# Optimization experiments

Measured on AMD Instinct MI355X. Metric: run time of the kernel, lower is better.

## Reference

```python
import jax, jax.numpy as jnp
import numpy as np

N = 25000          # nodes
E = 200000         # edges
MUL = 16           # multiplicity of 0e and 1o in irreps_in/out
NUM_RADIAL = 8
HIDDEN = 64
WNUMEL = 4 * MUL * MUL
PATH_ALPHA = 1.0 / np.sqrt(2.0 * MUL)   # 2 paths feed each output irrep, fan_in=MUL each
INV_SQRT3 = 1.0 / np.sqrt(3.0)          # CG coeff for 1o x 1o -> 0e (component norm)


def setup_inputs() -> dict:
    key = jax.random.key(0)
    ks = jax.random.split(key, 9)
    x = jax.random.normal(ks[0], (N, 4 * MUL), jnp.float32)          # [N, 64] = 16x0e + 16x1o
    edge_attr = jax.random.normal(ks[1], (E, 4), jnp.float32)        # [E, 4]  = 1x0e + 1x1o sh
    edge_length = jax.random.uniform(ks[2], (E,), jnp.float32, 0.0, 5.0)
    edge_src = jax.random.randint(ks[3], (E,), 0, N)
    edge_dst = jax.random.randint(ks[4], (E,), 0, N)
    W1 = jax.random.normal(ks[5], (NUM_RADIAL, HIDDEN), jnp.float32)
    W2 = jax.random.normal(ks[6], (HIDDEN, WNUMEL), jnp.float32)
    L0 = jax.random.normal(ks[7], (MUL, MUL), jnp.float32)           # sc Linear on 0e block
    L1 = jax.random.normal(ks[8], (MUL, MUL), jnp.float32)           # sc Linear on 1o block
    return dict(x=x, edge_attr=edge_attr, edge_length=edge_length,
                edge_src=edge_src, edge_dst=edge_dst, W1=W1, W2=W2, L0=L0, L1=L1)


def reference(x, edge_attr, edge_length, edge_src, edge_dst, W1, W2, L0, L1):
    # ---- radial Gaussian basis (centers linspace(0,5,8), sigma=1) ----
    centers = jnp.linspace(0.0, 5.0, NUM_RADIAL).astype(x.dtype)
    d = edge_length[:, None] - centers[None, :]
    radial = jnp.exp(-0.5 * d * d)                                   # [E, 8]
    # ---- radial MLP -> per-edge TP weights (e3nn FullyConnectedNet, silu) ----
    h = jax.nn.silu(radial @ W1 * (1.0 / np.sqrt(NUM_RADIAL)))       # [E, 64]
    w = (h @ W2 * (1.0 / np.sqrt(HIDDEN))).reshape(E, 4, MUL, MUL)   # [E, 4, 16, 16]
    # ---- gather source node features, split into l=0 and l=1 parts ----
    xj = x[edge_src]                                                  # [E, 64]
    xj0 = xj[:, :MUL]                                                 # [E, 16]
    xj1 = xj[:, MUL:].reshape(E, MUL, 3)                              # [E, 16, 3]
    sh0 = edge_attr[:, 0]                                             # [E]
    sh1 = edge_attr[:, 1:4]                                           # [E, 3]
    # ---- FullyConnectedTensorProduct: 4 CG paths with per-edge weights ----
    m0 = (jnp.einsum('eu,euv->ev', xj0 * sh0[:, None], w[:, 0])
          + INV_SQRT3 * jnp.einsum('euk,ek,euv->ev', xj1, sh1, w[:, 1])) * PATH_ALPHA  # [E,16]
    m1 = (jnp.einsum('eu,ek,euv->evk', xj0, sh1, w[:, 2])
          + jnp.einsum('euk,e,euv->evk', xj1, sh0, w[:, 3])) * PATH_ALPHA              # [E,16,3]
    m_ij = jnp.concatenate([m0, m1.reshape(E, 3 * MUL)], axis=1)      # [E, 64]
    # ---- scatter-add messages to destination nodes ----
    m_i = jax.ops.segment_sum(m_ij, edge_dst, num_segments=N)        # [N, 64]
    # ---- residual self-connection: o3.Linear per-l mixing ----
    x0 = x[:, :MUL]
    x1 = x[:, MUL:].reshape(N, MUL, 3)
    sc0 = x0 @ L0
    sc1 = jnp.einsum('nuk,uv->nvk', x1, L1).reshape(N, 3 * MUL)
    sc = jnp.concatenate([sc0, sc1], axis=1) * (1.0 / np.sqrt(MUL))
    return m_i + sc
```

## Files before the change

kernel.cpp:

```cpp
#include <hip/hip_runtime.h>

#define N_NODES 25000
#define N_EDGES 200000

constexpr int ET = 32;
constexpr int NTILES = 6250;
constexpr int GRID = 512;
constexpr int PL = ET * 17;
constexpr int CTS = 36;

typedef __attribute__((ext_vector_type(8))) _Float16 half8;
typedef __attribute__((ext_vector_type(4))) _Float16 half4;
typedef __attribute__((ext_vector_type(4))) float float4v;

__device__ __forceinline__ void gl_lds16(const void* g, void* l) {
    __builtin_amdgcn_global_load_lds((const __attribute__((address_space(1))) void*)g,
                                     (__attribute__((address_space(3))) void*)l, 16, 0, 0);
}
__device__ __forceinline__ void gl_lds4(const void* g, void* l) {
    __builtin_amdgcn_global_load_lds((const __attribute__((address_space(1))) void*)g,
                                     (__attribute__((address_space(3))) void*)l, 4, 0, 0);
}

__global__ __launch_bounds__(512, 4) void fused_kernel(
    const float* __restrict__ x, const float* __restrict__ edge_attr,
    const float* __restrict__ edge_length, const int* __restrict__ edge_src,
    const int* __restrict__ edge_dst, const float* __restrict__ W1,
    const float* __restrict__ W2, const float* __restrict__ L0,
    const float* __restrict__ L1, float* __restrict__ out) {

    const int t = threadIdx.x;
    const int w = t >> 6;
    const int lane = t & 63;
    const int q = w >> 1;
    const int uh = w & 1;
    const int qm = t & 15;
    const int quad = (t >> 4) & 3;
    const int eL = t >> 4;
    const int uL = t & 15;

    __shared__ __attribute__((aligned(16))) _Float16 lds_h16[ET * 72];
    __shared__ __attribute__((aligned(16))) float lds_cfT[3][16][CTS];
    __shared__ __attribute__((aligned(16))) float lds_cf3T[3][16][CTS];
    __shared__ __attribute__((aligned(16))) float lds_xch[12 * PL];
    __shared__ __attribute__((aligned(16))) float lds_w1t[64 * 8];
    __shared__ __attribute__((aligned(16))) float l0[256], l1[256];
    __shared__ __attribute__((aligned(16))) float lds_xj[2][ET * 64];
    __shared__ __attribute__((aligned(16))) float lds_ea[2][ET * 4];
    __shared__ __attribute__((aligned(16))) float lds_len[2][ET];
    __shared__ __attribute__((aligned(16))) int   lds_dst[2][ET];
    __shared__ __attribute__((aligned(16))) int   lds_srcb[2][ET];

    half8 bfr[8][2];
    {
        float scale = 0.0220970869f;
        if (q == 1) scale *= 0.5773502692f;
        const int kr = quad * 8;
        #pragma unroll
        for (int up = 0; up < 8; ++up) {
            const int col = q * 256 + (uh * 8 + up) * 16 + qm;
            #pragma unroll
            for (int kf = 0; kf < 2; ++kf) {
                half8 f;
                #pragma unroll
                for (int j = 0; j < 8; ++j) {
                    const int k = kf * 32 + kr + j;
                    f[j] = (_Float16)(W2[k * 1024 + col] * scale);
                }
                bfr[up][kf] = f;
            }
        }
    }
    lds_w1t[(t & 63) * 8 + (t >> 6)] = W1[t];
    if (t < 256) l0[t] = L0[t];
    else         l1[t - 256] = L1[t - 256];

    int T = blockIdx.x;
    if (w == 0 && lane < ET) gl_lds4(edge_src + T * ET + lane, &lds_srcb[1][0]);
    __syncthreads();
    {
        const int e4 = (w << 2) + (lane >> 4);
        const int src = lds_srcb[1][e4];
        gl_lds16(x + src * 64 + (lane & 15) * 4, &lds_xj[0][w * 256]);
    }
    if (w == 0 && lane < ET) gl_lds16(edge_attr + 4 * (T * ET + lane), &lds_ea[0][0]);
    if (w == 1 && lane < ET) gl_lds4(edge_length + T * ET + lane, &lds_len[0][0]);
    if (w == 2 && lane < ET) gl_lds4(edge_dst + T * ET + lane, &lds_dst[0][0]);
    if (w == 3 && lane < ET) {
        const int Tn = (T + GRID < NTILES) ? T + GRID : T;
        gl_lds4(edge_src + Tn * ET + lane, &lds_srcb[0][0]);
    }

    {
        const bool is0 = lane < 16;
        const int qq = lane - 16;
        const int v = is0 ? lane : qq / 3;
        const int k = is0 ? 0 : qq - 3 * v;
        const float* mat = is0 ? l0 : l1;
        for (int n = blockIdx.x * 8 + w; n < N_NODES; n += GRID * 8) {
            const float xv = x[n * 64 + lane];
            float s = 0.f;
            #pragma unroll
            for (int u = 0; u < 16; ++u) {
                const int sel = is0 ? u : 16 + 3 * u + k;
                s = fmaf(__shfl(xv, sel), mat[u * 16 + v], s);
            }
            atomicAdd(out + n * 64 + lane, 0.25f * s);
        }
    }
    __syncthreads();

    int p = 0;
    while (true) {
        {
            const float sh0 = lds_ea[p][eL * 4 + 0];
            const float s1x = lds_ea[p][eL * 4 + 1];
            const float s1y = lds_ea[p][eL * 4 + 2];
            const float s1z = lds_ea[p][eL * 4 + 3];
            const float* xr = &lds_xj[p][eL * 64];
            const float xj0v = xr[uL];
            const float x0 = xr[16 + 3 * uL];
            const float x1 = xr[17 + 3 * uL];
            const float x2 = xr[18 + 3 * uL];
            lds_cfT[0][uL][eL] = xj0v * sh0;
            lds_cfT[1][uL][eL] = fmaf(x0, s1x, fmaf(x1, s1y, x2 * s1z));
            lds_cfT[2][uL][eL] = xj0v;
            lds_cf3T[0][uL][eL] = x0 * sh0;
            lds_cf3T[1][uL][eL] = x1 * sh0;
            lds_cf3T[2][uL][eL] = x2 * sh0;
            const int c0 = uL * 4;
            const float len = lds_len[p][eL];
            float rad[8];
            #pragma unroll
            for (int r = 0; r < 8; ++r) {
                const float d = len - 0.7142857143f * (float)r;
                rad[r] = __expf(-0.5f * d * d);
            }
            half4 hv;
            #pragma unroll
            for (int i = 0; i < 4; ++i) {
                const float4v wA = *(const float4v*)(&lds_w1t[(c0 + i) * 8]);
                const float4v wB = *(const float4v*)(&lds_w1t[(c0 + i) * 8 + 4]);
                float s = rad[0] * wA[0] + rad[1] * wA[1] + rad[2] * wA[2] + rad[3] * wA[3]
                        + rad[4] * wB[0] + rad[5] * wB[1] + rad[6] * wB[2] + rad[7] * wB[3];
                s *= 0.3535533906f;
                hv[i] = (_Float16)(s / (1.f + __expf(-s)));
            }
            *(half4*)(&lds_h16[eL * 72 + c0]) = hv;
        }

        __syncthreads();

        const int Tn = T + GRID;
        if (Tn < NTILES) {
            const int pn = p ^ 1;
            {
                const int e4 = (w << 2) + (lane >> 4);
                const int src = lds_srcb[p][e4];
                gl_lds16(x + src * 64 + (lane & 15) * 4, &lds_xj[pn][w * 256]);
            }
            if (w == 0 && lane < ET) gl_lds16(edge_attr + 4 * (Tn * ET + lane), &lds_ea[pn][0]);
            if (w == 1 && lane < ET) gl_lds4(edge_length + Tn * ET + lane, &lds_len[pn][0]);
            if (w == 2 && lane < ET) gl_lds4(edge_dst + Tn * ET + lane, &lds_dst[pn][0]);
            if (w == 3 && lane < ET) {
                const int T2 = (Tn + GRID < NTILES) ? Tn + GRID : Tn;
                gl_lds4(edge_src + T2 * ET + lane, &lds_srcb[pn][0]);
            }
        }

        half8 ah[2][2];
        #pragma unroll
        for (int mt = 0; mt < 2; ++mt)
            #pragma unroll
            for (int kf = 0; kf < 2; ++kf)
                ah[mt][kf] = *(const half8*)(&lds_h16[(mt * 16 + qm) * 72 + kf * 32 + quad * 8]);

        if (q < 3) {
            float4v C[2];
            C[0] = (float4v){0.f, 0.f, 0.f, 0.f};
            C[1] = (float4v){0.f, 0.f, 0.f, 0.f};
            #pragma unroll
            for (int up = 0; up < 8; ++up) {
                const int u = uh * 8 + up;
                #pragma unroll
                for (int mt = 0; mt < 2; ++mt) {
                    float4v au = __builtin_amdgcn_mfma_f32_16x16x32_f16(
                        ah[mt][0], bfr[up][0], (float4v){0.f, 0.f, 0.f, 0.f}, 0, 0, 0);
                    au = __builtin_amdgcn_mfma_f32_16x16x32_f16(
                        ah[mt][1], bfr[up][1], au, 0, 0, 0);
                    const float4v cr = *(const float4v*)(&lds_cfT[q][u][mt * 16 + quad * 4]);
                    C[mt] += au * cr;
                }
            }
            float* xb = &lds_xch[(q * 2 + uh) * PL];
            #pragma unroll
            for (int mt = 0; mt < 2; ++mt)
                #pragma unroll
                for (int r = 0; r < 4; ++r)
                    xb[(mt * 16 + quad * 4 + r) * 17 + qm] = C[mt][r];
        } else {
            float4v C3[3][2];
            #pragma unroll
            for (int k = 0; k < 3; ++k) {
                C3[k][0] = (float4v){0.f, 0.f, 0.f, 0.f};
                C3[k][1] = (float4v){0.f, 0.f, 0.f, 0.f};
            }
            #pragma unroll
            for (int up = 0; up < 8; ++up) {
                const int u = uh * 8 + up;
                #pragma unroll
                for (int mt = 0; mt < 2; ++mt) {
                    float4v au = __builtin_amdgcn_mfma_f32_16x16x32_f16(
                        ah[mt][0], bfr[up][0], (float4v){0.f, 0.f, 0.f, 0.f}, 0, 0, 0);
                    au = __builtin_amdgcn_mfma_f32_16x16x32_f16(
                        ah[mt][1], bfr[up][1], au, 0, 0, 0);
                    #pragma unroll
                    for (int k = 0; k < 3; ++k) {
                        const float4v ck = *(const float4v*)(&lds_cf3T[k][u][mt * 16 + quad * 4]);
                        C3[k][mt] += au * ck;
                    }
                }
            }
            #pragma unroll
            for (int k = 0; k < 3; ++k) {
                float* xb = &lds_xch[(6 + uh * 3 + k) * PL];
                #pragma unroll
                for (int mt = 0; mt < 2; ++mt)
                    #pragma unroll
                    for (int r = 0; r < 4; ++r)
                        xb[(mt * 16 + quad * 4 + r) * 17 + qm] = C3[k][mt][r];
            }
        }

        __syncthreads();

        #pragma unroll
        for (int i = 0; i < 4; ++i) {
            const int idx = t + 512 * i;
            const int e = idx >> 6, j = idx & 63;
            float val;
            if (j < 16) {
                val = (lds_xch[0 * PL + e * 17 + j] + lds_xch[1 * PL + e * 17 + j])
                    + (lds_xch[2 * PL + e * 17 + j] + lds_xch[3 * PL + e * 17 + j]);
            } else {
                const int qj = j - 16, v = qj / 3, k = qj - 3 * v;
                const float s2 = lds_xch[4 * PL + e * 17 + v] + lds_xch[5 * PL + e * 17 + v];
                const float s3 = lds_xch[(6 + k) * PL + e * 17 + v]
                               + lds_xch[(9 + k) * PL + e * 17 + v];
                val = fmaf(s2, lds_ea[p][e * 4 + 1 + k], s3);
            }
            atomicAdd(out + lds_dst[p][e] * 64 + j, val);
        }

        if (Tn >= NTILES) break;
        T = Tn;
        p ^= 1;
    }
}

extern "C" void kernel_launch(void* const* d_in, const int* in_sizes, int n_in,
                              void* d_out, int out_size, void* d_ws, size_t ws_size,
                              hipStream_t stream) {
    const float* x           = (const float*)d_in[0];
    const float* edge_attr   = (const float*)d_in[1];
    const float* edge_length = (const float*)d_in[2];
    const int*   edge_src    = (const int*)d_in[3];
    const int*   edge_dst    = (const int*)d_in[4];
    const float* W1          = (const float*)d_in[5];
    const float* W2          = (const float*)d_in[6];
    const float* L0          = (const float*)d_in[7];
    const float* L1          = (const float*)d_in[8];
    float* out = (float*)d_out;

    hipMemsetAsync(out, 0, (size_t)N_NODES * 64 * sizeof(float), stream);
    fused_kernel<<<GRID, 512, 0, stream>>>(
        x, edge_attr, edge_length, edge_src, edge_dst, W1, W2, L0, L1, out);
}
```

Measured before the change: 213.8 us.

## Triple-buffer edge tile prefetch and swizzle LDS layouts to cut bank conflicts

The kernel moves from double to triple buffering of the per-tile gathered node features and edge data, so the gather for tile T+2·GRID is issued while tile T is processed. It also rotates the u index per edge group (uS swizzle) when writing the coefficient and hidden buffers, and re-pads the exchange buffer row and plane strides, both to reduce LDS bank conflicts. The MFMA loops are reordered to load the A fragments per m-tile and keep fewer accumulators live, which lowers register pressure. In exchange the kernel uses more LDS and has more complex buffer-index bookkeeping, and both can limit occupancy.

```diff
diff --git a/kernel.cpp b/kernel.cpp
--- a/kernel.cpp
+++ b/kernel.cpp
@@ -6,7 +6,8 @@
 constexpr int ET = 32;
 constexpr int NTILES = 6250;
 constexpr int GRID = 512;
-constexpr int PL = ET * 17;
+constexpr int XPS = 584;
+constexpr int XRS = 18;
 constexpr int CTS = 36;
 
 typedef __attribute__((ext_vector_type(8))) _Float16 half8;
@@ -38,18 +39,19 @@
     const int quad = (t >> 4) & 3;
     const int eL = t >> 4;
     const int uL = t & 15;
+    const int uS = (uL + ((eL & 3) << 2)) & 15;
 
     __shared__ __attribute__((aligned(16))) _Float16 lds_h16[ET * 72];
     __shared__ __attribute__((aligned(16))) float lds_cfT[3][16][CTS];
     __shared__ __attribute__((aligned(16))) float lds_cf3T[3][16][CTS];
-    __shared__ __attribute__((aligned(16))) float lds_xch[12 * PL];
+    __shared__ __attribute__((aligned(16))) float lds_xch[12 * XPS];
     __shared__ __attribute__((aligned(16))) float lds_w1t[64 * 8];
     __shared__ __attribute__((aligned(16))) float l0[256], l1[256];
-    __shared__ __attribute__((aligned(16))) float lds_xj[2][ET * 64];
-    __shared__ __attribute__((aligned(16))) float lds_ea[2][ET * 4];
-    __shared__ __attribute__((aligned(16))) float lds_len[2][ET];
-    __shared__ __attribute__((aligned(16))) int   lds_dst[2][ET];
-    __shared__ __attribute__((aligned(16))) int   lds_srcb[2][ET];
+    __shared__ __attribute__((aligned(16))) float lds_xj[3][ET * 64];
+    __shared__ __attribute__((aligned(16))) float lds_ea[3][ET * 4];
+    __shared__ __attribute__((aligned(16))) float lds_len[3][ET];
+    __shared__ __attribute__((aligned(16))) int   lds_dst[3][ET];
+    __shared__ __attribute__((aligned(16))) int   lds_srcb[3][ET];
 
     half8 bfr[8][2];
     {
@@ -76,20 +78,22 @@
     else         l1[t - 256] = L1[t - 256];
 
     int T = blockIdx.x;
-    if (w == 0 && lane < ET) gl_lds4(edge_src + T * ET + lane, &lds_srcb[1][0]);
+    if (w == 0 && lane < ET) gl_lds4(edge_src + T * ET + lane, &lds_srcb[0][0]);
+    if (w == 1 && lane < ET) gl_lds4(edge_src + (T + GRID) * ET + lane, &lds_srcb[1][0]);
+    if (w == 2 && lane < ET) gl_lds4(edge_src + (T + 2 * GRID) * ET + lane, &lds_srcb[2][0]);
     __syncthreads();
     {
         const int e4 = (w << 2) + (lane >> 4);
-        const int src = lds_srcb[1][e4];
-        gl_lds16(x + src * 64 + (lane & 15) * 4, &lds_xj[0][w * 256]);
+        const int c4 = (lane & 15) * 4;
+        gl_lds16(x + lds_srcb[0][e4] * 64 + c4, &lds_xj[0][w * 256]);
+        gl_lds16(x + lds_srcb[1][e4] * 64 + c4, &lds_xj[1][w * 256]);
     }
     if (w == 0 && lane < ET) gl_lds16(edge_attr + 4 * (T * ET + lane), &lds_ea[0][0]);
     if (w == 1 && lane < ET) gl_lds4(edge_length + T * ET + lane, &lds_len[0][0]);
     if (w == 2 && lane < ET) gl_lds4(edge_dst + T * ET + lane, &lds_dst[0][0]);
-    if (w == 3 && lane < ET) {
-        const int Tn = (T + GRID < NTILES) ? T + GRID : T;
-        gl_lds4(edge_src + Tn * ET + lane, &lds_srcb[0][0]);
-    }
+    if (w == 3 && lane < ET) gl_lds16(edge_attr + 4 * ((T + GRID) * ET + lane), &lds_ea[1][0]);
+    if (w == 4 && lane < ET) gl_lds4(edge_length + (T + GRID) * ET + lane, &lds_len[1][0]);
+    if (w == 5 && lane < ET) gl_lds4(edge_dst + (T + GRID) * ET + lane, &lds_dst[1][0]);
 
     {
         const bool is0 = lane < 16;
@@ -118,17 +122,17 @@
             const float s1y = lds_ea[p][eL * 4 + 2];
             const float s1z = lds_ea[p][eL * 4 + 3];
             const float* xr = &lds_xj[p][eL * 64];
-            const float xj0v = xr[uL];
-            const float x0 = xr[16 + 3 * uL];
-            const float x1 = xr[17 + 3 * uL];
-            const float x2 = xr[18 + 3 * uL];
-            lds_cfT[0][uL][eL] = xj0v * sh0;
-            lds_cfT[1][uL][eL] = fmaf(x0, s1x, fmaf(x1, s1y, x2 * s1z));
-            lds_cfT[2][uL][eL] = xj0v;
-            lds_cf3T[0][uL][eL] = x0 * sh0;
-            lds_cf3T[1][uL][eL] = x1 * sh0;
-            lds_cf3T[2][uL][eL] = x2 * sh0;
-            const int c0 = uL * 4;
+            const float xj0v = xr[uS];
+            const float x0 = xr[16 + 3 * uS];
+            const float x1 = xr[17 + 3 * uS];
+            const float x2 = xr[18 + 3 * uS];
+            lds_cfT[0][uS][eL] = xj0v * sh0;
+            lds_cfT[1][uS][eL] = fmaf(x0, s1x, fmaf(x1, s1y, x2 * s1z));
+            lds_cfT[2][uS][eL] = xj0v;
+            lds_cf3T[0][uS][eL] = x0 * sh0;
+            lds_cf3T[1][uS][eL] = x1 * sh0;
+            lds_cf3T[2][uS][eL] = x2 * sh0;
+            const int c0 = uS * 4;
             const float len = lds_len[p][eL];
             float rad[8];
             #pragma unroll
@@ -151,84 +155,71 @@
 
         __syncthreads();
 
-        const int Tn = T + GRID;
-        if (Tn < NTILES) {
-            const int pn = p ^ 1;
+        const int T2 = T + 2 * GRID;
+        if (T2 < NTILES) {
+            const int p2 = (p + 2) % 3;
             {
                 const int e4 = (w << 2) + (lane >> 4);
-                const int src = lds_srcb[p][e4];
-                gl_lds16(x + src * 64 + (lane & 15) * 4, &lds_xj[pn][w * 256]);
-            }
-            if (w == 0 && lane < ET) gl_lds16(edge_attr + 4 * (Tn * ET + lane), &lds_ea[pn][0]);
-            if (w == 1 && lane < ET) gl_lds4(edge_length + Tn * ET + lane, &lds_len[pn][0]);
-            if (w == 2 && lane < ET) gl_lds4(edge_dst + Tn * ET + lane, &lds_dst[pn][0]);
+                const int src = lds_srcb[p2][e4];
+                gl_lds16(x + src * 64 + (lane & 15) * 4, &lds_xj[p2][w * 256]);
+            }
+            if (w == 0 && lane < ET) gl_lds16(edge_attr + 4 * (T2 * ET + lane), &lds_ea[p2][0]);
+            if (w == 1 && lane < ET) gl_lds4(edge_length + T2 * ET + lane, &lds_len[p2][0]);
+            if (w == 2 && lane < ET) gl_lds4(edge_dst + T2 * ET + lane, &lds_dst[p2][0]);
             if (w == 3 && lane < ET) {
-                const int T2 = (Tn + GRID < NTILES) ? Tn + GRID : Tn;
-                gl_lds4(edge_src + T2 * ET + lane, &lds_srcb[pn][0]);
-            }
-        }
-
-        half8 ah[2][2];
-        #pragma unroll
-        for (int mt = 0; mt < 2; ++mt)
-            #pragma unroll
-            for (int kf = 0; kf < 2; ++kf)
-                ah[mt][kf] = *(const half8*)(&lds_h16[(mt * 16 + qm) * 72 + kf * 32 + quad * 8]);
+                const int e3 = min((T + 3 * GRID) * ET + lane, N_EDGES - 1);
+                gl_lds4(edge_src + e3, &lds_srcb[p][0]);
+            }
+        }
 
         if (q < 3) {
-            float4v C[2];
-            C[0] = (float4v){0.f, 0.f, 0.f, 0.f};
-            C[1] = (float4v){0.f, 0.f, 0.f, 0.f};
-            #pragma unroll
-            for (int up = 0; up < 8; ++up) {
-                const int u = uh * 8 + up;
-                #pragma unroll
-                for (int mt = 0; mt < 2; ++mt) {
+            #pragma unroll
+            for (int mt = 0; mt < 2; ++mt) {
+                const half8 a0 = *(const half8*)(&lds_h16[(mt * 16 + qm) * 72 + quad * 8]);
+                const half8 a1 = *(const half8*)(&lds_h16[(mt * 16 + qm) * 72 + 32 + quad * 8]);
+                float4v C = (float4v){0.f, 0.f, 0.f, 0.f};
+                #pragma unroll
+                for (int up = 0; up < 8; ++up) {
+                    const int u = uh * 8 + up;
                     float4v au = __builtin_amdgcn_mfma_f32_16x16x32_f16(
-                        ah[mt][0], bfr[up][0], (float4v){0.f, 0.f, 0.f, 0.f}, 0, 0, 0);
-                    au = __builtin_amdgcn_mfma_f32_16x16x32_f16(
-                        ah[mt][1], bfr[up][1], au, 0, 0, 0);
+                        a0, bfr[up][0], (float4v){0.f, 0.f, 0.f, 0.f}, 0, 0, 0);
+                    au = __builtin_amdgcn_mfma_f32_16x16x32_f16(a1, bfr[up][1], au, 0, 0, 0);
                     const float4v cr = *(const float4v*)(&lds_cfT[q][u][mt * 16 + quad * 4]);
-                    C[mt] += au * cr;
-                }
-            }
-            float* xb = &lds_xch[(q * 2 + uh) * PL];
-            #pragma unroll
-            for (int mt = 0; mt < 2; ++mt)
+                    C += au * cr;
+                }
+                float* xb = &lds_xch[(q * 2 + uh) * XPS];
                 #pragma unroll
                 for (int r = 0; r < 4; ++r)
-                    xb[(mt * 16 + quad * 4 + r) * 17 + qm] = C[mt][r];
+                    xb[(mt * 16 + quad * 4 + r) * XRS + qm] = C[r];
+            }
         } else {
-            float4v C3[3][2];
-            #pragma unroll
-            for (int k = 0; k < 3; ++k) {
-                C3[k][0] = (float4v){0.f, 0.f, 0.f, 0.f};
-                C3[k][1] = (float4v){0.f, 0.f, 0.f, 0.f};
-            }
-            #pragma unroll
-            for (int up = 0; up < 8; ++up) {
-                const int u = uh * 8 + up;
-                #pragma unroll
-                for (int mt = 0; mt < 2; ++mt) {
+            #pragma unroll
+            for (int mt = 0; mt < 2; ++mt) {
+                const half8 a0 = *(const half8*)(&lds_h16[(mt * 16 + qm) * 72 + quad * 8]);
+                const half8 a1 = *(const half8*)(&lds_h16[(mt * 16 + qm) * 72 + 32 + quad * 8]);
+                float4v C3[3];
+                C3[0] = (float4v){0.f, 0.f, 0.f, 0.f};
+                C3[1] = (float4v){0.f, 0.f, 0.f, 0.f};
+                C3[2] = (float4v){0.f, 0.f, 0.f, 0.f};
+                #pragma unroll
+                for (int up = 0; up < 8; ++up) {
+                    const int u = uh * 8 + up;
                     float4v au = __builtin_amdgcn_mfma_f32_16x16x32_f16(
-                        ah[mt][0], bfr[up][0], (float4v){0.f, 0.f, 0.f, 0.f}, 0, 0, 0);
-                    au = __builtin_amdgcn_mfma_f32_16x16x32_f16(
-                        ah[mt][1], bfr[up][1], au, 0, 0, 0);
+                        a0, bfr[up][0], (float4v){0.f, 0.f, 0.f, 0.f}, 0, 0, 0);
+                    au = __builtin_amdgcn_mfma_f32_16x16x32_f16(a1, bfr[up][1], au, 0, 0, 0);
                     #pragma unroll
                     for (int k = 0; k < 3; ++k) {
                         const float4v ck = *(const float4v*)(&lds_cf3T[k][u][mt * 16 + quad * 4]);
-                        C3[k][mt] += au * ck;
+                        C3[k] += au * ck;
                     }
                 }
-            }
-            #pragma unroll
-            for (int k = 0; k < 3; ++k) {
-                float* xb = &lds_xch[(6 + uh * 3 + k) * PL];
-                #pragma unroll
-                for (int mt = 0; mt < 2; ++mt)
+                #pragma unroll
+                for (int k = 0; k < 3; ++k) {
+                    float* xb = &lds_xch[(6 + uh * 3 + k) * XPS];
                     #pragma unroll
                     for (int r = 0; r < 4; ++r)
-                        xb[(mt * 16 + quad * 4 + r) * 17 + qm] = C3[k][mt][r];
+                        xb[(mt * 16 + quad * 4 + r) * XRS + qm] = C3[k][r];
+                }
             }
         }
 
@@ -240,21 +231,22 @@
             const int e = idx >> 6, j = idx & 63;
             float val;
             if (j < 16) {
-                val = (lds_xch[0 * PL + e * 17 + j] + lds_xch[1 * PL + e * 17 + j])
-                    + (lds_xch[2 * PL + e * 17 + j] + lds_xch[3 * PL + e * 17 + j]);
+                val = (lds_xch[0 * XPS + e * XRS + j] + lds_xch[1 * XPS + e * XRS + j])
+                    + (lds_xch[2 * XPS + e * XRS + j] + lds_xch[3 * XPS + e * XRS + j]);
             } else {
                 const int qj = j - 16, v = qj / 3, k = qj - 3 * v;
-                const float s2 = lds_xch[4 * PL + e * 17 + v] + lds_xch[5 * PL + e * 17 + v];
-                const float s3 = lds_xch[(6 + k) * PL + e * 17 + v]
-                               + lds_xch[(9 + k) * PL + e * 17 + v];
+                const float s2 = lds_xch[4 * XPS + e * XRS + v] + lds_xch[5 * XPS + e * XRS + v];
+                const float s3 = lds_xch[(6 + k) * XPS + e * XRS + v]
+                               + lds_xch[(9 + k) * XPS + e * XRS + v];
                 val = fmaf(s2, lds_ea[p][e * 4 + 1 + k], s3);
             }
             atomicAdd(out + lds_dst[p][e] * 64 + j, val);
         }
 
+        const int Tn = T + GRID;
         if (Tn >= NTILES) break;
         T = Tn;
-        p ^= 1;
+        p = (p + 1) % 3;
     }
 }
 
```

After: 181.5 us. 15.1% less time.
